# Performance work log

Hardware: AMD Instinct MI355X
Metric: run time of the kernel (lower is better)

The kernel has to match this reference:

```python
import jax, jax.numpy as jnp
import numpy as np

NP_, NA_ = 100_000, 50_000
E_ = 200_000
IN, HID, OUT = 128, 128, 128
HEADS = 4
D = HID // HEADS
# (src_node_type, dst_node_type) for edge types: cites, writes, written_by
EDGE_SPECS = [(0, 0), (1, 0), (0, 1)]
N_TYPES = 2
N_LAYERS = 2


def _rand_edges(key, e, n_src, n_dst):
    k1, k2 = jax.random.split(key)
    return jnp.stack([jax.random.randint(k1, (e,), 0, n_src),
                      jax.random.randint(k2, (e,), 0, n_dst)]).astype(jnp.int64)


def setup_inputs() -> dict:
    key = jax.random.key(0)
    ks = jax.random.split(key, 24)
    s = 0.05
    inp = {
        "x_paper": jax.random.normal(ks[0], (NP_, IN), jnp.float32),
        "x_author": jax.random.normal(ks[1], (NA_, IN), jnp.float32),
        "e_cites": _rand_edges(ks[2], E_, NP_, NP_),
        "e_writes": _rand_edges(ks[3], E_, NA_, NP_),
        "e_written": _rand_edges(ks[4], E_, NP_, NA_),
        # per-node-type input projection
        "lin_W": jax.random.normal(ks[5], (N_TYPES, IN, HID), jnp.float32) * s,
        "lin_b": jnp.zeros((N_TYPES, HID), jnp.float32),
        # per-layer, per-node-type K/Q/V projections
        "k_W": jax.random.normal(ks[6], (N_LAYERS, N_TYPES, HID, HID), jnp.float32) * s,
        "k_b": jnp.zeros((N_LAYERS, N_TYPES, HID), jnp.float32),
        "q_W": jax.random.normal(ks[7], (N_LAYERS, N_TYPES, HID, HID), jnp.float32) * s,
        "q_b": jnp.zeros((N_LAYERS, N_TYPES, HID), jnp.float32),
        "v_W": jax.random.normal(ks[8], (N_LAYERS, N_TYPES, HID, HID), jnp.float32) * s,
        "v_b": jnp.zeros((N_LAYERS, N_TYPES, HID), jnp.float32),
        # per-layer, per-node-type output projection a_lin
        "a_W": jax.random.normal(ks[9], (N_LAYERS, N_TYPES, HID, OUT), jnp.float32) * s,
        "a_b": jnp.zeros((N_LAYERS, N_TYPES, OUT), jnp.float32),
        # per-layer, per-node-type skip gate logit
        "skip": jnp.ones((N_LAYERS, N_TYPES), jnp.float32),
        # per-layer, per-edge-type relation matrices and priors
        "a_rel": jax.random.normal(ks[10], (N_LAYERS, 3, HEADS, D, D), jnp.float32) * s,
        "m_rel": jax.random.normal(ks[11], (N_LAYERS, 3, HEADS, D, D), jnp.float32) * s,
        "p_rel": jnp.ones((N_LAYERS, 3, HEADS), jnp.float32),
    }
    return inp


def _seg_softmax(logits, idx, n):
    m = jax.ops.segment_max(logits, idx, num_segments=n)  # [n,H]
    e = jnp.exp(logits - m[idx])
    s = jax.ops.segment_sum(e, idx, num_segments=n)
    return e / s[idx]


def _hgt_conv(xs, edges, kW, kb, qW, qb, vW, vb, aW, ab, skip, a_rel, m_rel, p_rel):
    ks = [(x @ kW[t] + kb[t]).reshape(-1, HEADS, D) for t, x in enumerate(xs)]
    qs = [(x @ qW[t] + qb[t]).reshape(-1, HEADS, D) for t, x in enumerate(xs)]
    vs = [(x @ vW[t] + vb[t]).reshape(-1, HEADS, D) for t, x in enumerate(xs)]
    acc = [jnp.zeros((x.shape[0], HEADS, D), x.dtype) for x in xs]
    scale = 1.0 / np.sqrt(D).astype(np.float32)
    for et, (s_t, d_t) in enumerate(EDGE_SPECS):
        src, dst = edges[et][0], edges[et][1]
        # relation-specific transform on the (smaller) node set, then gather
        kt = jnp.einsum('nhd,hde->nhe', ks[s_t], a_rel[et])
        vt = jnp.einsum('nhd,hde->nhe', vs[s_t], m_rel[et])
        n_dst = xs[d_t].shape[0]
        logits = (qs[d_t][dst] * kt[src]).sum(-1) * p_rel[et] * scale  # [E,H]
        att = _seg_softmax(logits, dst, n_dst)  # edge softmax per dst node (per edge type)
        msg = vt[src] * att[:, :, None]  # [E,H,D]
        acc[d_t] = acc[d_t] + jax.ops.segment_sum(msg, dst, num_segments=n_dst)
    outs = []
    for t, x in enumerate(xs):
        o = jax.nn.gelu(acc[t].reshape(x.shape[0], HID), approximate=False) @ aW[t] + ab[t]
        g = jax.nn.sigmoid(skip[t])  # out dim == in dim -> skip gate active
        outs.append(g * o + (1.0 - g) * x)
    return outs


def reference(x_paper, x_author, e_cites, e_writes, e_written,
              lin_W, lin_b, k_W, k_b, q_W, q_b, v_W, v_b,
              a_W, a_b, skip, a_rel, m_rel, p_rel):
    edges = [e_cites, e_writes, e_written]
    xs = [x_paper @ lin_W[0] + lin_b[0], x_author @ lin_W[1] + lin_b[1]]
    for L in range(N_LAYERS):
        xs = _hgt_conv(xs, edges, k_W[L], k_b[L], q_W[L], q_b[L], v_W[L], v_b[L],
                       a_W[L], a_b[L], skip[L], a_rel[L], m_rel[L], p_rel[L])
    return jnp.concatenate(xs, axis=0)  # [NP_+NA_, OUT]
```

## Files before the change

kernel.cpp:

```cpp
#include <hip/hip_runtime.h>
#include <math.h>

#define NPn 100000
#define NAn 50000
#define NTn 150000
#define En  200000
#define SCAN_N 250000

typedef short s16x8 __attribute__((ext_vector_type(8)));
typedef float f32x4 __attribute__((ext_vector_type(4)));

__device__ __forceinline__ unsigned short f2bfbits(float f) {
  unsigned u = __builtin_bit_cast(unsigned, f);
  return (unsigned short)((u + 0x7fffu + ((u >> 16) & 1u)) >> 16);
}
__device__ __forceinline__ float bf2f(unsigned short b) {
  return __builtin_bit_cast(float, (unsigned)b << 16);
}
__device__ __forceinline__ float gelu_f(float v) {
  return 0.5f * v * (1.f + erff(v * 0.70710678118654752f));
}

__global__ __launch_bounds__(256) void hist3_k(const int* __restrict__ e0, const int* __restrict__ e1,
                                               const int* __restrict__ e2, int* __restrict__ deg) {
  int i = blockIdx.x * 256 + threadIdx.x;
  int et = blockIdx.y;
  if (i >= En) return;
  const int* d = et == 0 ? e0 : (et == 1 ? e1 : e2);
  int etoff = et == 0 ? 0 : (et == 1 ? 100000 : 200000);
  atomicAdd(&deg[etoff + d[En + i]], 1);
}

__global__ __launch_bounds__(256) void scan1_k(const int* __restrict__ deg, int* __restrict__ bsum) {
  int t = threadIdx.x, lane = t & 63, wv = t >> 6;
  int base = blockIdx.x * 1024 + t * 4;
  int a0 = 0, a1 = 0, a2 = 0, a3 = 0;
  if (base + 3 < SCAN_N) {
    int4 v = *reinterpret_cast<const int4*>(deg + base);
    a0 = v.x; a1 = v.y; a2 = v.z; a3 = v.w;
  } else {
    if (base + 0 < SCAN_N) a0 = deg[base + 0];
    if (base + 1 < SCAN_N) a1 = deg[base + 1];
    if (base + 2 < SCAN_N) a2 = deg[base + 2];
    if (base + 3 < SCAN_N) a3 = deg[base + 3];
  }
  int s = a0 + a1 + a2 + a3;
  #pragma unroll
  for (int d = 1; d < 64; d <<= 1) s += __shfl_xor(s, d);
  __shared__ int wt[4];
  if (lane == 0) wt[wv] = s;
  __syncthreads();
  if (t == 0) bsum[blockIdx.x] = wt[0] + wt[1] + wt[2] + wt[3];
}

__global__ __launch_bounds__(256) void scan2_k(int* __restrict__ bsum, int nb) {
  int t = threadIdx.x, lane = t & 63, wv = t >> 6;
  int v = (t < nb) ? bsum[t] : 0;
  int x = v;
  #pragma unroll
  for (int d = 1; d < 64; d <<= 1) {
    int y = __shfl_up(x, d);
    if (lane >= d) x += y;
  }
  __shared__ int wt[4];
  if (lane == 63) wt[wv] = x;
  __syncthreads();
  int off = 0;
  for (int w = 0; w < wv; ++w) off += wt[w];
  if (t < nb) bsum[t] = x + off - v;
}

__global__ __launch_bounds__(256) void scan3_k(const int* __restrict__ deg, const int* __restrict__ bpre,
                                               int* __restrict__ S) {
  int t = threadIdx.x, lane = t & 63, wv = t >> 6;
  int base = blockIdx.x * 1024 + t * 4;
  int a[4] = {0, 0, 0, 0};
  if (base + 3 < SCAN_N) {
    int4 v = *reinterpret_cast<const int4*>(deg + base);
    a[0] = v.x; a[1] = v.y; a[2] = v.z; a[3] = v.w;
  } else {
    #pragma unroll
    for (int j = 0; j < 4; ++j) if (base + j < SCAN_N) a[j] = deg[base + j];
  }
  int s = a[0] + a[1] + a[2] + a[3];
  int x = s;
  #pragma unroll
  for (int d = 1; d < 64; d <<= 1) {
    int y = __shfl_up(x, d);
    if (lane >= d) x += y;
  }
  __shared__ int wt[4];
  if (lane == 63) wt[wv] = x;
  __syncthreads();
  int off = bpre[blockIdx.x];
  for (int w = 0; w < wv; ++w) off += wt[w];
  int ex = off + x - s;
  #pragma unroll
  for (int j = 0; j < 4; ++j) {
    int idx = base + j;
    if (idx < SCAN_N) {
      S[idx] = ex;
      ex += a[j];
      if (idx == SCAN_N - 1) S[SCAN_N] = ex;
    }
  }
}

__global__ __launch_bounds__(256) void fill3_k(const int* __restrict__ e0, const int* __restrict__ e1,
                                               const int* __restrict__ e2, int* cur, int* __restrict__ col) {
  int i = blockIdx.x * 256 + threadIdx.x;
  int et = blockIdx.y;
  if (i >= En) return;
  const int* ep = et == 0 ? e0 : (et == 1 ? e1 : e2);
  int etoff = et == 0 ? 0 : (et == 1 ? 100000 : 200000);
  int p = atomicAdd(&cur[etoff + ep[En + i]], 1);
  col[p] = ep[i];
}

__global__ __launch_bounds__(256) void fuse_k(const float* __restrict__ kW, const float* __restrict__ kb,
                                              const float* __restrict__ vW, const float* __restrict__ vb,
                                              const float* __restrict__ a_rel, const float* __restrict__ m_rel,
                                              float* __restrict__ Wf, float* __restrict__ bfv) {
  int b = blockIdx.x;
  int L = b / 6, et = (b % 6) / 2, which = b & 1;
  int s_t = (et == 1) ? 1 : 0;
  const float* W = which ? vW : kW;
  const float* bb = which ? vb : kb;
  const float* R = which ? m_rel : a_rel;
  const float* Wsrc = W + (size_t)(L * 2 + s_t) * 128 * 128;
  const float* bsrc = bb + (size_t)(L * 2 + s_t) * 128;
  const float* Rsrc = R + (size_t)(L * 3 + et) * 4 * 32 * 32;
  float* Wdst = Wf + (size_t)b * 128 * 128;
  float* bdst = bfv + (size_t)b * 128;
  for (int idx = threadIdx.x; idx < 128 * 128; idx += 256) {
    int i = idx >> 7, c = idx & 127;
    int h = c >> 5, cc = c & 31;
    const float* r = Rsrc + (size_t)h * 32 * 32 + cc;
    const float* w = Wsrc + (size_t)i * 128 + h * 32;
    float s = 0.f;
    #pragma unroll 8
    for (int d = 0; d < 32; ++d) s += w[d] * r[d * 32];
    Wdst[idx] = s;
  }
  for (int c = threadIdx.x; c < 128; c += 256) {
    int h = c >> 5, cc = c & 31;
    float s = 0.f;
    for (int d = 0; d < 32; ++d) s += bsrc[h * 32 + d] * Rsrc[((size_t)h * 32 + d) * 32 + cc];
    bdst[c] = s;
  }
}

__global__ __launch_bounds__(256) void pack_k(const float* __restrict__ linW, const float* __restrict__ qW,
                                              const float* __restrict__ aW, const float* __restrict__ Wf,
                                              unsigned short* __restrict__ Wp) {
  int m = blockIdx.x;
  const float* src;
  if (m < 2) src = linW + (size_t)m * 16384;
  else if (m < 6) src = qW + (size_t)(m - 2) * 16384;
  else if (m < 18) src = Wf + (size_t)(m - 6) * 16384;
  else src = aW + (size_t)(m - 18) * 16384;
  int lane = threadIdx.x & 63, wv = threadIdx.x >> 6;
  unsigned short* dst = Wp + (size_t)m * 16384;
  for (int ct = 0; ct < 8; ++ct) {
    s16x8 t;
    #pragma unroll
    for (int i = 0; i < 8; ++i) {
      int k = wv * 32 + (lane >> 4) * 8 + i;
      int n = ct * 16 + (lane & 15);
      t[i] = (short)f2bfbits(src[k * 128 + n]);
    }
    *reinterpret_cast<s16x8*>(dst + ((size_t)(wv * 8 + ct) * 64 + lane) * 8) = t;
  }
}

struct IJob { const float* X; const unsigned short* W; const float* bias; unsigned short* Y; int N; };

__global__ __launch_bounds__(256, 2) void iproj_k(IJob ja, IJob jb) {
  IJob j = blockIdx.y ? jb : ja;
  int ntj = (j.N + 63) >> 6;
  int tile = blockIdx.x;
  if (tile >= ntj) return;
  int lane = threadIdx.x & 63, wv = threadIdx.x >> 6;
  int rowsLeft = j.N - tile * 64;

  __shared__ float xin[64 * 128];
  {
    const uint4* src = reinterpret_cast<const uint4*>(j.X + (size_t)tile * 64 * 128);
    uint4* dst = reinterpret_cast<uint4*>(xin);
    for (int c = threadIdx.x; c < 2048; c += 256) {
      int row = c >> 5;
      if (row < rowsLeft) dst[c] = src[c];
    }
  }
  __syncthreads();

  int lr = wv * 16 + (lane & 15);
  s16x8 af[4];
  #pragma unroll
  for (int ks = 0; ks < 4; ++ks) {
    const float* p = xin + lr * 128 + (lane >> 4) * 8 + ks * 32;
    s16x8 t;
    #pragma unroll
    for (int i = 0; i < 8; ++i) t[i] = (short)f2bfbits(p[i]);
    af[ks] = t;
  }

  s16x8 bfr[4][8];
  #pragma unroll
  for (int ks = 0; ks < 4; ++ks)
    #pragma unroll
    for (int ct = 0; ct < 8; ++ct)
      bfr[ks][ct] = *reinterpret_cast<const s16x8*>(j.W + ((size_t)(ks * 8 + ct) * 64 + lane) * 8);

  float bias_[8];
  #pragma unroll
  for (int ct = 0; ct < 8; ++ct) bias_[ct] = j.bias[ct * 16 + (lane & 15)];

  f32x4 acc[8];
  #pragma unroll
  for (int ct = 0; ct < 8; ++ct) acc[ct] = (f32x4){0.f, 0.f, 0.f, 0.f};
  #pragma unroll
  for (int ks = 0; ks < 4; ++ks)
    #pragma unroll
    for (int ct = 0; ct < 8; ++ct)
      acc[ct] = __builtin_amdgcn_mfma_f32_16x16x32_bf16(af[ks], bfr[ks][ct], acc[ct], 0, 0, 0);

  __syncthreads();
  unsigned short* ot = reinterpret_cast<unsigned short*>(xin);
  int c0 = lane & 15, r00 = wv * 16 + (lane >> 4) * 4;
  #pragma unroll
  for (int ct = 0; ct < 8; ++ct)
    #pragma unroll
    for (int i = 0; i < 4; ++i)
      ot[(r00 + i) * 128 + ct * 16 + c0] = f2bfbits(acc[ct][i] + bias_[ct]);
  __syncthreads();
  {
    const uint4* src = reinterpret_cast<const uint4*>(ot);
    uint4* dst = reinterpret_cast<uint4*>(j.Y + (size_t)tile * 64 * 128);
    for (int c = threadIdx.x; c < 1024; c += 256) {
      int row = c >> 4;
      if (row < rowsLeft) dst[c] = src[c];
    }
  }
}

struct QKVJob {
  const unsigned short* X; int N; int nm; int pad;
  const unsigned short* W[5];
  const float* bias[5];
  unsigned short* Y[5];
};

__global__ __launch_bounds__(256, 2) void qkv_k(QKVJob ja, QKVJob jb) {
  QKVJob j = blockIdx.y ? jb : ja;
  int ntj = (j.N + 63) >> 6;
  int tile = blockIdx.x;
  if (tile >= ntj) return;
  int lane = threadIdx.x & 63, wv = threadIdx.x >> 6;
  int rowsLeft = j.N - tile * 64;

  int arow = tile * 64 + wv * 16 + (lane & 15);
  if (arow >= j.N) arow = j.N - 1;
  const unsigned short* xp = j.X + (size_t)arow * 128 + (lane >> 4) * 8;
  s16x8 af[4];
  #pragma unroll
  for (int ks = 0; ks < 4; ++ks) af[ks] = *reinterpret_cast<const s16x8*>(xp + ks * 32);

  __shared__ unsigned short ot[64 * 128];
  int c0 = lane & 15, r00 = wv * 16 + (lane >> 4) * 4;

  for (int m = 0; m < j.nm; ++m) {
    s16x8 bfr[4][8];
    #pragma unroll
    for (int ks = 0; ks < 4; ++ks)
      #pragma unroll
      for (int ct = 0; ct < 8; ++ct)
        bfr[ks][ct] = *reinterpret_cast<const s16x8*>(j.W[m] + ((size_t)(ks * 8 + ct) * 64 + lane) * 8);
    float bias_[8];
    #pragma unroll
    for (int ct = 0; ct < 8; ++ct) bias_[ct] = j.bias[m][ct * 16 + (lane & 15)];

    f32x4 acc[8];
    #pragma unroll
    for (int ct = 0; ct < 8; ++ct) acc[ct] = (f32x4){0.f, 0.f, 0.f, 0.f};
    #pragma unroll
    for (int ks = 0; ks < 4; ++ks)
      #pragma unroll
      for (int ct = 0; ct < 8; ++ct)
        acc[ct] = __builtin_amdgcn_mfma_f32_16x16x32_bf16(af[ks], bfr[ks][ct], acc[ct], 0, 0, 0);

    if (m) __syncthreads();
    #pragma unroll
    for (int ct = 0; ct < 8; ++ct)
      #pragma unroll
      for (int i = 0; i < 4; ++i)
        ot[(r00 + i) * 128 + ct * 16 + c0] = f2bfbits(acc[ct][i] + bias_[ct]);
    __syncthreads();
    const uint4* src = reinterpret_cast<const uint4*>(ot);
    uint4* dst = reinterpret_cast<uint4*>(j.Y[m] + (size_t)tile * 64 * 128);
    for (int c = threadIdx.x; c < 1024; c += 256) {
      int row = c >> 4;
      if (row < rowsLeft) dst[c] = src[c];
    }
  }
}

struct OJob {
  const unsigned short* G;
  const unsigned short* W;
  const float* bias;
  const unsigned short* skip;
  const float* skp;
  unsigned short* Yb;
  float* Yf;
  int N;
};

template <int FINAL>
__global__ __launch_bounds__(256, 2) void oproj_k(OJob ja, OJob jb) {
  OJob j = blockIdx.y ? jb : ja;
  int ntj = (j.N + 63) >> 6;
  int tile = blockIdx.x;
  if (tile >= ntj) return;
  int lane = threadIdx.x & 63, wv = threadIdx.x >> 6;
  int rowsLeft = j.N - tile * 64;

  __shared__ unsigned short sk[64 * 128];
  __shared__ float of[FINAL ? 64 * 128 : 1];
  {
    const uint4* src = reinterpret_cast<const uint4*>(j.skip + (size_t)tile * 64 * 128);
    uint4* dst = reinterpret_cast<uint4*>(sk);
    for (int c = threadIdx.x; c < 1024; c += 256) {
      int row = c >> 4;
      if (row < rowsLeft) dst[c] = src[c];
    }
  }

  int arow = tile * 64 + wv * 16 + (lane & 15);
  if (arow >= j.N) arow = j.N - 1;
  const unsigned short* xp = j.G + (size_t)arow * 128 + (lane >> 4) * 8;
  s16x8 af[4];
  #pragma unroll
  for (int ks = 0; ks < 4; ++ks) af[ks] = *reinterpret_cast<const s16x8*>(xp + ks * 32);

  s16x8 bfr[4][8];
  #pragma unroll
  for (int ks = 0; ks < 4; ++ks)
    #pragma unroll
    for (int ct = 0; ct < 8; ++ct)
      bfr[ks][ct] = *reinterpret_cast<const s16x8*>(j.W + ((size_t)(ks * 8 + ct) * 64 + lane) * 8);
  float bias_[8];
  #pragma unroll
  for (int ct = 0; ct < 8; ++ct) bias_[ct] = j.bias[ct * 16 + (lane & 15)];
  float g = 1.f / (1.f + __expf(-*j.skp));

  f32x4 acc[8];
  #pragma unroll
  for (int ct = 0; ct < 8; ++ct) acc[ct] = (f32x4){0.f, 0.f, 0.f, 0.f};
  #pragma unroll
  for (int ks = 0; ks < 4; ++ks)
    #pragma unroll
    for (int ct = 0; ct < 8; ++ct)
      acc[ct] = __builtin_amdgcn_mfma_f32_16x16x32_bf16(af[ks], bfr[ks][ct], acc[ct], 0, 0, 0);

  __syncthreads();
  int c0 = lane & 15, r00 = wv * 16 + (lane >> 4) * 4;
  #pragma unroll
  for (int ct = 0; ct < 8; ++ct)
    #pragma unroll
    for (int i = 0; i < 4; ++i) {
      int idx = (r00 + i) * 128 + ct * 16 + c0;
      float y = g * (acc[ct][i] + bias_[ct]) + (1.f - g) * bf2f(sk[idx]);
      if (FINAL) of[idx] = y;
      else sk[idx] = f2bfbits(y);
    }
  __syncthreads();
  if (FINAL) {
    const uint4* src = reinterpret_cast<const uint4*>(of);
    uint4* dst = reinterpret_cast<uint4*>(j.Yf + (size_t)tile * 64 * 128);
    for (int c = threadIdx.x; c < 2048; c += 256) {
      int row = c >> 5;
      if (row < rowsLeft) dst[c] = src[c];
    }
  } else {
    const uint4* src = reinterpret_cast<const uint4*>(sk);
    uint4* dst = reinterpret_cast<uint4*>(j.Yb + (size_t)tile * 64 * 128);
    for (int c = threadIdx.x; c < 1024; c += 256) {
      int row = c >> 4;
      if (row < rowsLeft) dst[c] = src[c];
    }
  }
}

template <int NPARTS>
__global__ __launch_bounds__(256) void attn_k(const int* __restrict__ S, const int* __restrict__ col,
                                              const unsigned short* __restrict__ kt,
                                              const unsigned short* __restrict__ vt,
                                              const unsigned short* __restrict__ qb,
                                              unsigned short* __restrict__ gbuf,
                                              const float* __restrict__ prp0, const float* __restrict__ prp1,
                                              int n_dst, int qbase, int soff0, int soff1,
                                              int ktbase0, int ktbase1) {
  int node = (blockIdx.x * 256 + threadIdx.x) >> 6;
  if (node >= n_dst) return;
  int lane = threadIdx.x & 63;
  int h = lane >> 4;

  ushort2 qv = *reinterpret_cast<const ushort2*>(qb + (size_t)(qbase + node) * 128 + lane * 2);
  float q0 = bf2f(qv.x), q1 = bf2f(qv.y);

  float facc0 = 0.f, facc1 = 0.f;
  #pragma unroll
  for (int p = 0; p < NPARTS; ++p) {
    int soff = p ? soff1 : soff0;
    const unsigned short* ktb = kt + (size_t)(p ? ktbase1 : ktbase0) * 128;
    const unsigned short* vtb = vt + (size_t)(p ? ktbase1 : ktbase0) * 128;
    const float* prp = p ? prp1 : prp0;
    float pr = prp[h] * 0.17677669529663687f;
    int rs = S[soff + node], re = S[soff + node + 1];
    if (rs < re) {
      float m = -3.0e38f, den = 0.f, n0 = 0.f, n1 = 0.f;
      for (int i = rs; i < re; ++i) {
        int s = col[i];
        ushort2 kv = *reinterpret_cast<const ushort2*>(ktb + (size_t)s * 128 + lane * 2);
        float pdot = q0 * bf2f(kv.x) + q1 * bf2f(kv.y);
        pdot += __shfl_xor(pdot, 1); pdot += __shfl_xor(pdot, 2);
        pdot += __shfl_xor(pdot, 4); pdot += __shfl_xor(pdot, 8);
        float pm = pdot * pr;
        ushort2 vv = *reinterpret_cast<const ushort2*>(vtb + (size_t)s * 128 + lane * 2);
        float nm = fmaxf(m, pm);
        float sc = __expf(m - nm);
        float w = __expf(pm - nm);
        den = den * sc + w;
        n0 = n0 * sc + w * bf2f(vv.x);
        n1 = n1 * sc + w * bf2f(vv.y);
        m = nm;
      }
      float inv = 1.f / den;
      facc0 += n0 * inv;
      facc1 += n1 * inv;
    }
  }
  ushort2 o;
  o.x = f2bfbits(gelu_f(facc0));
  o.y = f2bfbits(gelu_f(facc1));
  *reinterpret_cast<ushort2*>(gbuf + (size_t)(qbase + node) * 128 + lane * 2) = o;
}

extern "C" void kernel_launch(void* const* d_in, const int* in_sizes, int n_in,
                              void* d_out, int out_size, void* d_ws, size_t ws_size,
                              hipStream_t stream) {
  const float* x_paper  = (const float*)d_in[0];
  const float* x_author = (const float*)d_in[1];
  const int* e[3] = {(const int*)d_in[2], (const int*)d_in[3], (const int*)d_in[4]};
  const float* linW = (const float*)d_in[5];
  const float* linb = (const float*)d_in[6];
  const float* kW = (const float*)d_in[7];
  const float* kb = (const float*)d_in[8];
  const float* qW = (const float*)d_in[9];
  const float* qbv = (const float*)d_in[10];
  const float* vW = (const float*)d_in[11];
  const float* vb = (const float*)d_in[12];
  const float* aW = (const float*)d_in[13];
  const float* ab = (const float*)d_in[14];
  const float* skipv = (const float*)d_in[15];
  const float* a_rel = (const float*)d_in[16];
  const float* m_rel = (const float*)d_in[17];
  const float* prel  = (const float*)d_in[18];

  char* ws = (char*)d_ws;
  size_t off = 0;
  auto alloc = [&](size_t b) { char* p = ws + off; off = (off + b + 255) & ~(size_t)255; return p; };
  unsigned short* qbuf = (unsigned short*)alloc((size_t)NTn * 128 * 2);
  unsigned short* ktA  = (unsigned short*)alloc((size_t)SCAN_N * 128 * 2);
  unsigned short* vtA  = (unsigned short*)alloc((size_t)SCAN_N * 128 * 2);
  unsigned short* gbuf = (unsigned short*)alloc((size_t)NTn * 128 * 2);
  unsigned short* xb   = (unsigned short*)alloc((size_t)NTn * 128 * 2);
  int* deg   = (int*)alloc((size_t)SCAN_N * 4);
  int* cur   = (int*)alloc((size_t)SCAN_N * 4);
  int* S     = (int*)alloc((size_t)(SCAN_N + 1) * 4);
  int* bsum  = (int*)alloc(256 * 4);
  int* col   = (int*)alloc((size_t)3 * En * 4);
  float* Wf  = (float*)alloc((size_t)12 * 16384 * 4);
  float* bfv = (float*)alloc((size_t)12 * 128 * 4);
  unsigned short* Wp = (unsigned short*)alloc((size_t)22 * 16384 * 2);

  hipMemsetAsync(deg, 0, (size_t)SCAN_N * 4, stream);
  hist3_k<<<dim3(782, 3), 256, 0, stream>>>(e[0], e[1], e[2], deg);
  scan1_k<<<245, 256, 0, stream>>>(deg, bsum);
  scan2_k<<<1, 256, 0, stream>>>(bsum, 245);
  scan3_k<<<245, 256, 0, stream>>>(deg, bsum, S);
  hipMemcpyAsync(cur, S, (size_t)SCAN_N * 4, hipMemcpyDeviceToDevice, stream);
  fill3_k<<<dim3(782, 3), 256, 0, stream>>>(e[0], e[1], e[2], cur, col);

  fuse_k<<<12, 256, 0, stream>>>(kW, kb, vW, vb, a_rel, m_rel, Wf, bfv);
  pack_k<<<22, 256, 0, stream>>>(linW, qW, aW, Wf, Wp);

  const dim3 gg(1563, 2);

  {
    IJob jp  = {x_paper,  Wp + 0 * 16384, linb,        xb,                       NPn};
    IJob jat = {x_author, Wp + 1 * 16384, linb + 128,  xb + (size_t)NPn * 128,   NAn};
    iproj_k<<<gg, 256, 0, stream>>>(jp, jat);
  }

  const int ktbases[3] = {0, 100000, 150000};

  for (int L = 0; L < 2; ++L) {
    {
      QKVJob jp{}, jat{};
      jp.X = xb; jp.N = NPn; jp.nm = 5;
      jp.W[0] = Wp + (size_t)(2 + L * 2) * 16384;      jp.bias[0] = qbv + (L * 2) * 128;            jp.Y[0] = qbuf;
      jp.W[1] = Wp + (size_t)(6 + L * 6 + 0) * 16384;  jp.bias[1] = bfv + (size_t)(L * 6 + 0) * 128; jp.Y[1] = ktA + (size_t)ktbases[0] * 128;
      jp.W[2] = Wp + (size_t)(6 + L * 6 + 1) * 16384;  jp.bias[2] = bfv + (size_t)(L * 6 + 1) * 128; jp.Y[2] = vtA + (size_t)ktbases[0] * 128;
      jp.W[3] = Wp + (size_t)(6 + L * 6 + 4) * 16384;  jp.bias[3] = bfv + (size_t)(L * 6 + 4) * 128; jp.Y[3] = ktA + (size_t)ktbases[2] * 128;
      jp.W[4] = Wp + (size_t)(6 + L * 6 + 5) * 16384;  jp.bias[4] = bfv + (size_t)(L * 6 + 5) * 128; jp.Y[4] = vtA + (size_t)ktbases[2] * 128;
      jat.X = xb + (size_t)NPn * 128; jat.N = NAn; jat.nm = 3;
      jat.W[0] = Wp + (size_t)(3 + L * 2) * 16384;     jat.bias[0] = qbv + (L * 2 + 1) * 128;        jat.Y[0] = qbuf + (size_t)NPn * 128;
      jat.W[1] = Wp + (size_t)(6 + L * 6 + 2) * 16384; jat.bias[1] = bfv + (size_t)(L * 6 + 2) * 128; jat.Y[1] = ktA + (size_t)ktbases[1] * 128;
      jat.W[2] = Wp + (size_t)(6 + L * 6 + 3) * 16384; jat.bias[2] = bfv + (size_t)(L * 6 + 3) * 128; jat.Y[2] = vtA + (size_t)ktbases[1] * 128;
      qkv_k<<<gg, 256, 0, stream>>>(jp, jat);
    }
    attn_k<2><<<25000, 256, 0, stream>>>(S, col, ktA, vtA, qbuf, gbuf,
                                         prel + (size_t)(L * 3 + 0) * 4, prel + (size_t)(L * 3 + 1) * 4,
                                         NPn, 0, 0, 100000, ktbases[0], ktbases[1]);
    attn_k<1><<<12500, 256, 0, stream>>>(S, col, ktA, vtA, qbuf, gbuf,
                                         prel + (size_t)(L * 3 + 2) * 4, nullptr,
                                         NAn, NPn, 200000, 0, ktbases[2], 0);
    {
      OJob jp  = {gbuf, Wp + (size_t)(18 + L * 2) * 16384, ab + (L * 2) * 128,
                  xb, skipv + L * 2, xb, (float*)d_out, NPn};
      OJob jat = {gbuf + (size_t)NPn * 128, Wp + (size_t)(19 + L * 2) * 16384, ab + (L * 2 + 1) * 128,
                  xb + (size_t)NPn * 128, skipv + L * 2 + 1, xb + (size_t)NPn * 128,
                  (float*)d_out + (size_t)NPn * 128, NAn};
      if (L == 0) oproj_k<0><<<gg, 256, 0, stream>>>(jp, jat);
      else        oproj_k<1><<<gg, 256, 0, stream>>>(jp, jat);
    }
  }
}
```

Measured before the change: 706.5 us.

## Stage GEMM weights in LDS, pad tiles, double-tile QKV with weight prefetch

```diff
diff --git a/kernel.cpp b/kernel.cpp
--- a/kernel.cpp
+++ b/kernel.cpp
@@ -175,22 +175,29 @@
 
 struct IJob { const float* X; const unsigned short* W; const float* bias; unsigned short* Y; int N; };
 
-__global__ __launch_bounds__(256, 2) void iproj_k(IJob ja, IJob jb) {
+__global__ __launch_bounds__(256) void iproj_k(IJob ja, IJob jb) {
   IJob j = blockIdx.y ? jb : ja;
   int ntj = (j.N + 63) >> 6;
   int tile = blockIdx.x;
   if (tile >= ntj) return;
   int lane = threadIdx.x & 63, wv = threadIdx.x >> 6;
-  int rowsLeft = j.N - tile * 64;
-
-  __shared__ float xin[64 * 128];
+  int t = threadIdx.x;
+  int rl = j.N - tile * 64; if (rl > 64) rl = 64;
+
+  __shared__ float xin[64 * 132];
+  __shared__ unsigned short wlds[16384];
+
   {
     const uint4* src = reinterpret_cast<const uint4*>(j.X + (size_t)tile * 64 * 128);
     uint4* dst = reinterpret_cast<uint4*>(xin);
-    for (int c = threadIdx.x; c < 2048; c += 256) {
+    for (int c = t; c < 2048; c += 256) {
       int row = c >> 5;
-      if (row < rowsLeft) dst[c] = src[c];
-    }
+      if (row < rl) dst[row * 33 + (c & 31)] = src[c];
+    }
+    const uint4* ws4 = reinterpret_cast<const uint4*>(j.W);
+    uint4* wl4 = reinterpret_cast<uint4*>(wlds);
+    #pragma unroll
+    for (int i = 0; i < 8; ++i) wl4[i * 256 + t] = ws4[i * 256 + t];
   }
   __syncthreads();
 
@@ -198,32 +205,27 @@
   s16x8 af[4];
   #pragma unroll
   for (int ks = 0; ks < 4; ++ks) {
-    const float* p = xin + lr * 128 + (lane >> 4) * 8 + ks * 32;
-    s16x8 t;
-    #pragma unroll
-    for (int i = 0; i < 8; ++i) t[i] = (short)f2bfbits(p[i]);
-    af[ks] = t;
-  }
-
-  s16x8 bfr[4][8];
+    const float* p = xin + lr * 132 + (lane >> 4) * 8 + ks * 32;
+    s16x8 tt;
+    #pragma unroll
+    for (int i = 0; i < 8; ++i) tt[i] = (short)f2bfbits(p[i]);
+    af[ks] = tt;
+  }
+
+  float bias_[8];
+  #pragma unroll
+  for (int ct = 0; ct < 8; ++ct) bias_[ct] = j.bias[ct * 16 + (lane & 15)];
+
+  f32x4 acc[8];
+  #pragma unroll
+  for (int ct = 0; ct < 8; ++ct) acc[ct] = (f32x4){0.f, 0.f, 0.f, 0.f};
   #pragma unroll
   for (int ks = 0; ks < 4; ++ks)
     #pragma unroll
-    for (int ct = 0; ct < 8; ++ct)
-      bfr[ks][ct] = *reinterpret_cast<const s16x8*>(j.W + ((size_t)(ks * 8 + ct) * 64 + lane) * 8);
-
-  float bias_[8];
-  #pragma unroll
-  for (int ct = 0; ct < 8; ++ct) bias_[ct] = j.bias[ct * 16 + (lane & 15)];
-
-  f32x4 acc[8];
-  #pragma unroll
-  for (int ct = 0; ct < 8; ++ct) acc[ct] = (f32x4){0.f, 0.f, 0.f, 0.f};
-  #pragma unroll
-  for (int ks = 0; ks < 4; ++ks)
-    #pragma unroll
-    for (int ct = 0; ct < 8; ++ct)
-      acc[ct] = __builtin_amdgcn_mfma_f32_16x16x32_bf16(af[ks], bfr[ks][ct], acc[ct], 0, 0, 0);
+    for (int ct = 0; ct < 8; ++ct) {
+      s16x8 b = *reinterpret_cast<const s16x8*>(wlds + ((size_t)(ks * 8 + ct) * 64 + lane) * 8);
+      acc[ct] = __builtin_amdgcn_mfma_f32_16x16x32_bf16(af[ks], b, acc[ct], 0, 0, 0);
+    }
 
   __syncthreads();
   unsigned short* ot = reinterpret_cast<unsigned short*>(xin);
@@ -232,14 +234,13 @@
   for (int ct = 0; ct < 8; ++ct)
     #pragma unroll
     for (int i = 0; i < 4; ++i)
-      ot[(r00 + i) * 128 + ct * 16 + c0] = f2bfbits(acc[ct][i] + bias_[ct]);
+      ot[(r00 + i) * 132 + ct * 16 + c0] = f2bfbits(acc[ct][i] + bias_[ct]);
   __syncthreads();
   {
-    const uint4* src = reinterpret_cast<const uint4*>(ot);
-    uint4* dst = reinterpret_cast<uint4*>(j.Y + (size_t)tile * 64 * 128);
-    for (int c = threadIdx.x; c < 1024; c += 256) {
-      int row = c >> 4;
-      if (row < rowsLeft) dst[c] = src[c];
+    unsigned int* dstU = reinterpret_cast<unsigned int*>(j.Y + (size_t)tile * 64 * 128);
+    for (int c = t; c < 4096; c += 256) {
+      int row = c >> 6, col2 = c & 63;
+      if (row < rl) dstU[row * 64 + col2] = *reinterpret_cast<const unsigned int*>(ot + row * 132 + col2 * 2);
     }
   }
 }
@@ -251,56 +252,78 @@
   unsigned short* Y[5];
 };
 
-__global__ __launch_bounds__(256, 2) void qkv_k(QKVJob ja, QKVJob jb) {
+__global__ __launch_bounds__(256) void qkv_k(QKVJob ja, QKVJob jb) {
   QKVJob j = blockIdx.y ? jb : ja;
-  int ntj = (j.N + 63) >> 6;
+  int ntj = (j.N + 127) >> 7;
   int tile = blockIdx.x;
   if (tile >= ntj) return;
   int lane = threadIdx.x & 63, wv = threadIdx.x >> 6;
-  int rowsLeft = j.N - tile * 64;
-
-  int arow = tile * 64 + wv * 16 + (lane & 15);
-  if (arow >= j.N) arow = j.N - 1;
-  const unsigned short* xp = j.X + (size_t)arow * 128 + (lane >> 4) * 8;
-  s16x8 af[4];
-  #pragma unroll
-  for (int ks = 0; ks < 4; ++ks) af[ks] = *reinterpret_cast<const s16x8*>(xp + ks * 32);
-
-  __shared__ unsigned short ot[64 * 128];
-  int c0 = lane & 15, r00 = wv * 16 + (lane >> 4) * 4;
+  int t = threadIdx.x;
+  int nst = j.N - tile * 128 > 64 ? 2 : 1;
+
+  __shared__ unsigned short wlds[16384];
+  __shared__ unsigned short ot[64 * 132];
+
+  s16x8 af[2][4];
+  #pragma unroll
+  for (int st = 0; st < 2; ++st) {
+    int arow = tile * 128 + st * 64 + wv * 16 + (lane & 15);
+    if (arow >= j.N) arow = j.N - 1;
+    const unsigned short* xp = j.X + (size_t)arow * 128 + (lane >> 4) * 8;
+    #pragma unroll
+    for (int ks = 0; ks < 4; ++ks) af[st][ks] = *reinterpret_cast<const s16x8*>(xp + ks * 32);
+  }
+
+  uint4 wpend[8];
+  {
+    const uint4* ws4 = reinterpret_cast<const uint4*>(j.W[0]);
+    #pragma unroll
+    for (int i = 0; i < 8; ++i) wpend[i] = ws4[i * 256 + t];
+  }
 
   for (int m = 0; m < j.nm; ++m) {
-    s16x8 bfr[4][8];
-    #pragma unroll
-    for (int ks = 0; ks < 4; ++ks)
+    __syncthreads();
+    {
+      uint4* wl4 = reinterpret_cast<uint4*>(wlds);
+      #pragma unroll
+      for (int i = 0; i < 8; ++i) wl4[i * 256 + t] = wpend[i];
+    }
+    __syncthreads();
+    if (m + 1 < j.nm) {
+      const uint4* wn = reinterpret_cast<const uint4*>(j.W[m + 1]);
+      #pragma unroll
+      for (int i = 0; i < 8; ++i) wpend[i] = wn[i * 256 + t];
+    }
+    float bias_[8];
+    #pragma unroll
+    for (int ct = 0; ct < 8; ++ct) bias_[ct] = j.bias[m][ct * 16 + (lane & 15)];
+
+    for (int st = 0; st < nst; ++st) {
+      f32x4 acc[8];
+      #pragma unroll
+      for (int ct = 0; ct < 8; ++ct) acc[ct] = (f32x4){0.f, 0.f, 0.f, 0.f};
+      #pragma unroll
+      for (int ks = 0; ks < 4; ++ks)
+        #pragma unroll
+        for (int ct = 0; ct < 8; ++ct) {
+          s16x8 b = *reinterpret_cast<const s16x8*>(wlds + ((size_t)(ks * 8 + ct) * 64 + lane) * 8);
+          acc[ct] = __builtin_amdgcn_mfma_f32_16x16x32_bf16(af[st][ks], b, acc[ct], 0, 0, 0);
+        }
+
+      if (st) __syncthreads();
+      int c0 = lane & 15, r00 = wv * 16 + (lane >> 4) * 4;
       #pragma unroll
       for (int ct = 0; ct < 8; ++ct)
-        bfr[ks][ct] = *reinterpret_cast<const s16x8*>(j.W[m] + ((size_t)(ks * 8 + ct) * 64 + lane) * 8);
-    float bias_[8];
-    #pragma unroll
-    for (int ct = 0; ct < 8; ++ct) bias_[ct] = j.bias[m][ct * 16 + (lane & 15)];
-
-    f32x4 acc[8];
-    #pragma unroll
-    for (int ct = 0; ct < 8; ++ct) acc[ct] = (f32x4){0.f, 0.f, 0.f, 0.f};
-    #pragma unroll
-    for (int ks = 0; ks < 4; ++ks)
-      #pragma unroll
-      for (int ct = 0; ct < 8; ++ct)
-        acc[ct] = __builtin_amdgcn_mfma_f32_16x16x32_bf16(af[ks], bfr[ks][ct], acc[ct], 0, 0, 0);
-
-    if (m) __syncthreads();
-    #pragma unroll
-    for (int ct = 0; ct < 8; ++ct)
-      #pragma unroll
-      for (int i = 0; i < 4; ++i)
-        ot[(r00 + i) * 128 + ct * 16 + c0] = f2bfbits(acc[ct][i] + bias_[ct]);
-    __syncthreads();
-    const uint4* src = reinterpret_cast<const uint4*>(ot);
-    uint4* dst = reinterpret_cast<uint4*>(j.Y[m] + (size_t)tile * 64 * 128);
-    for (int c = threadIdx.x; c < 1024; c += 256) {
-      int row = c >> 4;
-      if (row < rowsLeft) dst[c] = src[c];
+        #pragma unroll
+        for (int i = 0; i < 4; ++i)
+          ot[(r00 + i) * 132 + ct * 16 + c0] = f2bfbits(acc[ct][i] + bias_[ct]);
+      __syncthreads();
+      int rl = j.N - (tile * 128 + st * 64); if (rl > 64) rl = 64;
+      unsigned int* dstU = reinterpret_cast<unsigned int*>(j.Y[m] + ((size_t)tile * 128 + st * 64) * 128);
+      for (int c = t; c < 4096; c += 256) {
+        int row = c >> 6, col2 = c & 63;
+        if (row < rl) dstU[row * 64 + col2] = *reinterpret_cast<const unsigned int*>(ot + row * 132 + col2 * 2);
+      }
     }
   }
 }
@@ -317,22 +340,27 @@
 };
 
 template <int FINAL>
-__global__ __launch_bounds__(256, 2) void oproj_k(OJob ja, OJob jb) {
+__global__ __launch_bounds__(256) void oproj_k(OJob ja, OJob jb) {
   OJob j = blockIdx.y ? jb : ja;
   int ntj = (j.N + 63) >> 6;
   int tile = blockIdx.x;
   if (tile >= ntj) return;
   int lane = threadIdx.x & 63, wv = threadIdx.x >> 6;
-  int rowsLeft = j.N - tile * 64;
-
-  __shared__ unsigned short sk[64 * 128];
-  __shared__ float of[FINAL ? 64 * 128 : 1];
+  int t = threadIdx.x;
+  int rl = j.N - tile * 64; if (rl > 64) rl = 64;
+
+  __shared__ unsigned short wlds[16384];
+  __shared__ unsigned short sk[64 * 132];
+
   {
-    const uint4* src = reinterpret_cast<const uint4*>(j.skip + (size_t)tile * 64 * 128);
-    uint4* dst = reinterpret_cast<uint4*>(sk);
-    for (int c = threadIdx.x; c < 1024; c += 256) {
-      int row = c >> 4;
-      if (row < rowsLeft) dst[c] = src[c];
+    const uint4* ws4 = reinterpret_cast<const uint4*>(j.W);
+    uint4* wl4 = reinterpret_cast<uint4*>(wlds);
+    #pragma unroll
+    for (int i = 0; i < 8; ++i) wl4[i * 256 + t] = ws4[i * 256 + t];
+    const unsigned int* srcU = reinterpret_cast<const unsigned int*>(j.skip + (size_t)tile * 64 * 128);
+    for (int c = t; c < 4096; c += 256) {
+      int row = c >> 6, col2 = c & 63;
+      if (row < rl) *reinterpret_cast<unsigned int*>(sk + row * 132 + col2 * 2) = srcU[row * 64 + col2];
     }
   }
 
@@ -343,51 +371,52 @@
   #pragma unroll
   for (int ks = 0; ks < 4; ++ks) af[ks] = *reinterpret_cast<const s16x8*>(xp + ks * 32);
 
-  s16x8 bfr[4][8];
-  #pragma unroll
-  for (int ks = 0; ks < 4; ++ks)
-    #pragma unroll
-    for (int ct = 0; ct < 8; ++ct)
-      bfr[ks][ct] = *reinterpret_cast<const s16x8*>(j.W + ((size_t)(ks * 8 + ct) * 64 + lane) * 8);
   float bias_[8];
   #pragma unroll
   for (int ct = 0; ct < 8; ++ct) bias_[ct] = j.bias[ct * 16 + (lane & 15)];
   float g = 1.f / (1.f + __expf(-*j.skp));
 
+  __syncthreads();
+
   f32x4 acc[8];
   #pragma unroll
   for (int ct = 0; ct < 8; ++ct) acc[ct] = (f32x4){0.f, 0.f, 0.f, 0.f};
   #pragma unroll
   for (int ks = 0; ks < 4; ++ks)
     #pragma unroll
+    for (int ct = 0; ct < 8; ++ct) {
+      s16x8 b = *reinterpret_cast<const s16x8*>(wlds + ((size_t)(ks * 8 + ct) * 64 + lane) * 8);
+      acc[ct] = __builtin_amdgcn_mfma_f32_16x16x32_bf16(af[ks], b, acc[ct], 0, 0, 0);
+    }
+
+  int c0 = lane & 15, r00 = wv * 16 + (lane >> 4) * 4;
+  if (FINAL) {
+    float* yf = j.Yf + (size_t)tile * 64 * 128;
+    #pragma unroll
     for (int ct = 0; ct < 8; ++ct)
-      acc[ct] = __builtin_amdgcn_mfma_f32_16x16x32_bf16(af[ks], bfr[ks][ct], acc[ct], 0, 0, 0);
-
-  __syncthreads();
-  int c0 = lane & 15, r00 = wv * 16 + (lane >> 4) * 4;
-  #pragma unroll
-  for (int ct = 0; ct < 8; ++ct)
-    #pragma unroll
-    for (int i = 0; i < 4; ++i) {
-      int idx = (r00 + i) * 128 + ct * 16 + c0;
-      float y = g * (acc[ct][i] + bias_[ct]) + (1.f - g) * bf2f(sk[idx]);
-      if (FINAL) of[idx] = y;
-      else sk[idx] = f2bfbits(y);
-    }
-  __syncthreads();
-  if (FINAL) {
-    const uint4* src = reinterpret_cast<const uint4*>(of);
-    uint4* dst = reinterpret_cast<uint4*>(j.Yf + (size_t)tile * 64 * 128);
-    for (int c = threadIdx.x; c < 2048; c += 256) {
-      int row = c >> 5;
-      if (row < rowsLeft) dst[c] = src[c];
-    }
+      #pragma unroll
+      for (int i = 0; i < 4; ++i) {
+        int r = r00 + i;
+        if (r < rl) {
+          int idx = r * 132 + ct * 16 + c0;
+          float y = g * (acc[ct][i] + bias_[ct]) + (1.f - g) * bf2f(sk[idx]);
+          yf[r * 128 + ct * 16 + c0] = y;
+        }
+      }
   } else {
-    const uint4* src = reinterpret_cast<const uint4*>(sk);
-    uint4* dst = reinterpret_cast<uint4*>(j.Yb + (size_t)tile * 64 * 128);
-    for (int c = threadIdx.x; c < 1024; c += 256) {
-      int row = c >> 4;
-      if (row < rowsLeft) dst[c] = src[c];
+    #pragma unroll
+    for (int ct = 0; ct < 8; ++ct)
+      #pragma unroll
+      for (int i = 0; i < 4; ++i) {
+        int idx = (r00 + i) * 132 + ct * 16 + c0;
+        float y = g * (acc[ct][i] + bias_[ct]) + (1.f - g) * bf2f(sk[idx]);
+        sk[idx] = f2bfbits(y);
+      }
+    __syncthreads();
+    unsigned int* dstU = reinterpret_cast<unsigned int*>(j.Yb + (size_t)tile * 64 * 128);
+    for (int c = t; c < 4096; c += 256) {
+      int row = c >> 6, col2 = c & 63;
+      if (row < rl) dstU[row * 64 + col2] = *reinterpret_cast<const unsigned int*>(sk + row * 132 + col2 * 2);
     }
   }
 }
@@ -496,12 +525,10 @@
   fuse_k<<<12, 256, 0, stream>>>(kW, kb, vW, vb, a_rel, m_rel, Wf, bfv);
   pack_k<<<22, 256, 0, stream>>>(linW, qW, aW, Wf, Wp);
 
-  const dim3 gg(1563, 2);
-
   {
     IJob jp  = {x_paper,  Wp + 0 * 16384, linb,        xb,                       NPn};
     IJob jat = {x_author, Wp + 1 * 16384, linb + 128,  xb + (size_t)NPn * 128,   NAn};
-    iproj_k<<<gg, 256, 0, stream>>>(jp, jat);
+    iproj_k<<<dim3(1563, 2), 256, 0, stream>>>(jp, jat);
   }
 
   const int ktbases[3] = {0, 100000, 150000};
@@ -510,16 +537,16 @@
     {
       QKVJob jp{}, jat{};
       jp.X = xb; jp.N = NPn; jp.nm = 5;
-      jp.W[0] = Wp + (size_t)(2 + L * 2) * 16384;      jp.bias[0] = qbv + (L * 2) * 128;            jp.Y[0] = qbuf;
+      jp.W[0] = Wp + (size_t)(2 + L * 2) * 16384;      jp.bias[0] = qbv + (L * 2) * 128;             jp.Y[0] = qbuf;
       jp.W[1] = Wp + (size_t)(6 + L * 6 + 0) * 16384;  jp.bias[1] = bfv + (size_t)(L * 6 + 0) * 128; jp.Y[1] = ktA + (size_t)ktbases[0] * 128;
       jp.W[2] = Wp + (size_t)(6 + L * 6 + 1) * 16384;  jp.bias[2] = bfv + (size_t)(L * 6 + 1) * 128; jp.Y[2] = vtA + (size_t)ktbases[0] * 128;
       jp.W[3] = Wp + (size_t)(6 + L * 6 + 4) * 16384;  jp.bias[3] = bfv + (size_t)(L * 6 + 4) * 128; jp.Y[3] = ktA + (size_t)ktbases[2] * 128;
       jp.W[4] = Wp + (size_t)(6 + L * 6 + 5) * 16384;  jp.bias[4] = bfv + (size_t)(L * 6 + 5) * 128; jp.Y[4] = vtA + (size_t)ktbases[2] * 128;
       jat.X = xb + (size_t)NPn * 128; jat.N = NAn; jat.nm = 3;
-      jat.W[0] = Wp + (size_t)(3 + L * 2) * 16384;     jat.bias[0] = qbv + (L * 2 + 1) * 128;        jat.Y[0] = qbuf + (size_t)NPn * 128;
+      jat.W[0] = Wp + (size_t)(3 + L * 2) * 16384;     jat.bias[0] = qbv + (L * 2 + 1) * 128;         jat.Y[0] = qbuf + (size_t)NPn * 128;
       jat.W[1] = Wp + (size_t)(6 + L * 6 + 2) * 16384; jat.bias[1] = bfv + (size_t)(L * 6 + 2) * 128; jat.Y[1] = ktA + (size_t)ktbases[1] * 128;
       jat.W[2] = Wp + (size_t)(6 + L * 6 + 3) * 16384; jat.bias[2] = bfv + (size_t)(L * 6 + 3) * 128; jat.Y[2] = vtA + (size_t)ktbases[1] * 128;
-      qkv_k<<<gg, 256, 0, stream>>>(jp, jat);
+      qkv_k<<<dim3(782, 2), 256, 0, stream>>>(jp, jat);
     }
     attn_k<2><<<25000, 256, 0, stream>>>(S, col, ktA, vtA, qbuf, gbuf,
                                          prel + (size_t)(L * 3 + 0) * 4, prel + (size_t)(L * 3 + 1) * 4,
@@ -533,8 +560,8 @@
       OJob jat = {gbuf + (size_t)NPn * 128, Wp + (size_t)(19 + L * 2) * 16384, ab + (L * 2 + 1) * 128,
                   xb + (size_t)NPn * 128, skipv + L * 2 + 1, xb + (size_t)NPn * 128,
                   (float*)d_out + (size_t)NPn * 128, NAn};
-      if (L == 0) oproj_k<0><<<gg, 256, 0, stream>>>(jp, jat);
-      else        oproj_k<1><<<gg, 256, 0, stream>>>(jp, jat);
-    }
-  }
-}
+      if (L == 0) oproj_k<0><<<dim3(1563, 2), 256, 0, stream>>>(jp, jat);
+      else        oproj_k<1><<<dim3(1563, 2), 256, 0, stream>>>(jp, jat);
+    }
+  }
+}
```

Result: slower. 860.8 us (+21.8%).
